# Kernel tuning notes

Hardware: AMD Instinct MI355X
Metric: run time of the kernel (lower is better)

The kernel has to match this reference:

```python
import jax, jax.numpy as jnp
import numpy as np

B, N, E = 8, 50000, 400000
DIMS = [4, 64, 64, 3]
K = 3
EPS = 1e-5
NEG_SLOPE = 0.01


def _gcn_norm(edge_index, num_nodes):
    # TAGConv uses gcn_norm with unit edge weights and add_self_loops=False.
    row, col = edge_index[0], edge_index[1]
    w = jnp.ones(row.shape[0], dtype=jnp.float32)
    deg = jax.ops.segment_sum(w, col, num_segments=num_nodes)  # in-degree at target
    dis = jnp.where(deg > 0, jnp.power(jnp.maximum(deg, 1.0), -0.5), 0.0)
    return dis[row] * dis[col]  # [E]


def _tag_conv(x, W, b, row, col, norm, num_nodes):
    # x: [B, N, Fin]; W: [K+1, Fin, Fout]; b: [Fout]
    out = jnp.einsum('bnf,fg->bng', x, W[0])
    h = x
    for k in range(1, W.shape[0]):
        msg = h[:, row, :] * norm[None, :, None]            # [B, E, Fin] gather
        h = jnp.zeros((x.shape[0], num_nodes, x.shape[2]), x.dtype).at[:, col, :].add(msg)  # scatter-add
        out = out + jnp.einsum('bnf,fg->bng', h, W[k])
    return out + b


def _batchnorm(x2d, gamma, beta):
    # training-mode BatchNorm1d over batch dim (biased variance, eps=1e-5)
    mean = jnp.mean(x2d, axis=0)
    var = jnp.mean(jnp.square(x2d - mean), axis=0)
    return gamma * (x2d - mean) * jax.lax.rsqrt(var + EPS) + beta


def _leaky_relu(x):
    return jnp.where(x >= 0, x, NEG_SLOPE * x)


def setup_inputs() -> dict:
    key = jax.random.key(0)
    ks = jax.random.split(key, 12)
    inp = {}
    inp['x'] = jax.random.normal(ks[0], (B, N, DIMS[0]), dtype=jnp.float32)
    inp['edge_index'] = jax.random.randint(ks[1], (2, E), 0, N, dtype=jnp.int64)
    inp['val_min'] = jax.random.uniform(ks[2], (N, 3), dtype=jnp.float32) - 1.5
    inp['val_max'] = jax.random.uniform(ks[3], (N, 3), dtype=jnp.float32) + 0.5
    for l in range(3):
        fin, fout = DIMS[l], DIMS[l + 1]
        scale = 1.0 / np.sqrt(fin)
        inp[f'W{l}'] = jax.random.uniform(ks[4 + l], (K + 1, fin, fout), minval=-scale, maxval=scale, dtype=jnp.float32)
        inp[f'b{l}'] = jnp.zeros((fout,), jnp.float32)
    for l in range(2):
        inp[f'gamma{l}'] = jnp.ones((N * DIMS[l + 1],), jnp.float32)
        inp[f'beta{l}'] = jnp.zeros((N * DIMS[l + 1],), jnp.float32)
    return inp


def reference(x, edge_index, val_min, val_max, W0, b0, W1, b1, W2, b2,
              gamma0, beta0, gamma1, beta1):
    row, col = edge_index[0], edge_index[1]
    norm = _gcn_norm(edge_index, N)
    Ws = [W0, W1, W2]
    bs = [b0, b1, b2]
    gammas = [gamma0, gamma1]
    betas = [beta0, beta1]
    out = x
    for layer in range(2):  # num_layers - 1 hidden layers
        out = _tag_conv(out, Ws[layer], bs[layer], row, col, norm, N)
        d = DIMS[layer + 1]
        out = _batchnorm(out.reshape(-1, N * d), gammas[layer], betas[layer]).reshape(-1, N, d)
        out = _leaky_relu(out)
    out = _tag_conv(out, Ws[2], bs[2], row, col, norm, N)  # [B, N, 3]
    # non_linearity: gamma = min + (max - min) / (1 + exp(U))
    return val_min[None] + (val_max - val_min)[None] / (1.0 + jnp.exp(out))
```

## Files before the change

### kernel.cpp

```cpp
#include <hip/hip_runtime.h>
#include <math.h>

constexpr int B = 8;
constexpr int N = 50000;
constexpr int E = 400000;
constexpr int NH = 25000;
constexpr float BN_EPS = 1e-5f;
constexpr float NEG = 0.01f;


__device__ __forceinline__ unsigned clamp_src(int s) {
    unsigned u = (unsigned)s;
    return (u < (unsigned)N) ? u : 0u;
}

__device__ __forceinline__ unsigned pack_bf16(float a, float b) {
    unsigned ua = __float_as_uint(a);
    unsigned ub = __float_as_uint(b);
    ua = (ua + 0x7FFFu + ((ua >> 16) & 1u)) >> 16;
    ub = (ub + 0x7FFFu + ((ub >> 16) & 1u)) >> 16;
    return (ub << 16) | (ua & 0xFFFFu);
}
__device__ __forceinline__ float unpack_lo(unsigned u) { return __uint_as_float(u << 16); }
__device__ __forceinline__ float unpack_hi(unsigned u) { return __uint_as_float(u & 0xFFFF0000u); }

__device__ __forceinline__ void store_row64_bf(uint4* p, const float acc[64]) {
#pragma unroll
    for (int q = 0; q < 8; ++q) {
        uint4 v;
        v.x = pack_bf16(acc[q * 8 + 0], acc[q * 8 + 1]);
        v.y = pack_bf16(acc[q * 8 + 2], acc[q * 8 + 3]);
        v.z = pack_bf16(acc[q * 8 + 4], acc[q * 8 + 5]);
        v.w = pack_bf16(acc[q * 8 + 6], acc[q * 8 + 7]);
        p[q] = v;
    }
}


__global__ __launch_bounds__(256) void deg2_kernel(const int* __restrict__ row, const int* __restrict__ col,
                                                   float* __restrict__ deg, int* __restrict__ deg_lo) {
    int e = blockIdx.x * blockDim.x + threadIdx.x;
    if (e >= E) return;
    unsigned r = clamp_src(row[e]), c = clamp_src(col[e]);
    atomicAdd(&deg[c], 1.0f);
    if (r < (unsigned)NH) atomicAdd(&deg_lo[c], 1);
}

__global__ __launch_bounds__(256) void scan1_kernel(const float* __restrict__ deg,
                                                    int* __restrict__ part, int* __restrict__ bsum) {
    __shared__ int sm[4];
    int i = blockIdx.x * blockDim.x + threadIdx.x;
    int v = (i < N) ? (int)deg[i] : 0;
    int lane = threadIdx.x & 63, wv = threadIdx.x >> 6;
    int x = v;
#pragma unroll
    for (int off = 1; off < 64; off <<= 1) {
        int t = __shfl_up(x, off);
        if (lane >= off) x += t;
    }
    if (lane == 63) sm[wv] = x;
    __syncthreads();
    int add = 0;
#pragma unroll
    for (int w = 0; w < 4; ++w) if (w < wv) add += sm[w];
    if (i < N) part[i] = x - v + add;
    if (threadIdx.x == blockDim.x - 1) bsum[blockIdx.x] = x + add;
}

__global__ __launch_bounds__(256) void scan2_kernel(const int* __restrict__ bsum, int* __restrict__ boff,
                                                    int nb, int* __restrict__ rowptr) {
    __shared__ int sm[4];
    int i = threadIdx.x;
    int v = (i < nb) ? bsum[i] : 0;
    int lane = i & 63, wv = i >> 6;
    int x = v;
#pragma unroll
    for (int off = 1; off < 64; off <<= 1) {
        int t = __shfl_up(x, off);
        if (lane >= off) x += t;
    }
    if (lane == 63) sm[wv] = x;
    __syncthreads();
    int add = 0;
#pragma unroll
    for (int w = 0; w < 4; ++w) if (w < wv) add += sm[w];
    if (i < nb) boff[i] = x - v + add;
    if (i == 0) rowptr[N] = E;
}

__global__ __launch_bounds__(256) void scan3_kernel(const int* __restrict__ part, const int* __restrict__ boff,
                                                    int* __restrict__ rowptr) {
    int i = blockIdx.x * blockDim.x + threadIdx.x;
    if (i < N) rowptr[i] = part[i] + boff[blockIdx.x];
}

__global__ __launch_bounds__(256) void fill_kernel(const int* __restrict__ row, const int* __restrict__ col,
                                                   const int* __restrict__ rowptr, const int* __restrict__ deg_lo,
                                                   int* __restrict__ cur_lo, int* __restrict__ cur_hi,
                                                   int* __restrict__ csr_src) {
    int e = blockIdx.x * blockDim.x + threadIdx.x;
    if (e >= E) return;
    unsigned r = clamp_src(row[e]), c = clamp_src(col[e]);
    unsigned p;
    if (r < (unsigned)NH)
        p = (unsigned)(rowptr[c] + atomicAdd(&cur_lo[c], 1));
    else
        p = (unsigned)(rowptr[c] + deg_lo[c] + atomicAdd(&cur_hi[c], 1));
    if (p >= (unsigned)E) p = E - 1;
    csr_src[p] = (int)r;
}

__global__ __launch_bounds__(256) void dis_kernel(float* __restrict__ deg) {
    int i = blockIdx.x * blockDim.x + threadIdx.x;
    if (i < N) {
        float d = deg[i];
        deg[i] = (d > 0.f) ? rsqrtf(d) : 0.f;
    }
}


template<bool INBF>
__global__ __launch_bounds__(256) void xprop_kernel(const void* __restrict__ xin, const int* __restrict__ rowptr,
                                                    const int* __restrict__ csr_src, const float* __restrict__ dis,
                                                    uint2* __restrict__ xout) {
    int b = blockIdx.x & 7;
    int n = (blockIdx.x >> 3) * blockDim.x + threadIdx.x;
    if (n >= N) return;
    float a0 = 0.f, a1 = 0.f, a2 = 0.f, a3 = 0.f;
    int beg = rowptr[n], end = rowptr[n + 1];
    if (beg < 0) beg = 0;
    if (end > E) end = E;
    for (int i = beg; i < end; ++i) {
        unsigned s = clamp_src(csr_src[i]);
        float w = dis[s];
        if constexpr (!INBF) {
            float4 v = *((const float4*)xin + (size_t)b * N + s);
            a0 = fmaf(w, v.x, a0); a1 = fmaf(w, v.y, a1);
            a2 = fmaf(w, v.z, a2); a3 = fmaf(w, v.w, a3);
        } else {
            uint2 v = *((const uint2*)xin + (size_t)b * N + s);
            a0 = fmaf(w, unpack_lo(v.x), a0); a1 = fmaf(w, unpack_hi(v.x), a1);
            a2 = fmaf(w, unpack_lo(v.y), a2); a3 = fmaf(w, unpack_hi(v.y), a3);
        }
    }
    float dn = dis[n];
    uint2 o;
    o.x = pack_bf16(a0 * dn, a1 * dn);
    o.y = pack_bf16(a2 * dn, a3 * dn);
    xout[(size_t)b * N + n] = o;
}


__device__ __forceinline__ void load_xv(const float4* __restrict__ x0, const uint2* __restrict__ x1,
                                        const uint2* __restrict__ x2, const uint2* __restrict__ x3,
                                        size_t ro, float xv[16]) {
    float4 v = x0[ro];
    xv[0] = v.x; xv[1] = v.y; xv[2] = v.z; xv[3] = v.w;
    uint2 u1 = x1[ro], u2 = x2[ro], u3 = x3[ro];
    xv[4] = unpack_lo(u1.x); xv[5] = unpack_hi(u1.x); xv[6] = unpack_lo(u1.y); xv[7] = unpack_hi(u1.y);
    xv[8] = unpack_lo(u2.x); xv[9] = unpack_hi(u2.x); xv[10] = unpack_lo(u2.y); xv[11] = unpack_hi(u2.y);
    xv[12] = unpack_lo(u3.x); xv[13] = unpack_hi(u3.x); xv[14] = unpack_lo(u3.y); xv[15] = unpack_hi(u3.y);
}


__global__ __launch_bounds__(256) void build_h1_kernel(const float4* __restrict__ x0, const uint2* __restrict__ x1,
                                                       const uint2* __restrict__ x2, const uint2* __restrict__ x3,
                                                       const float* __restrict__ W0,
                                                       const float* __restrict__ gamma, const float* __restrict__ beta,
                                                       uint4* __restrict__ h1) {
    int gid = blockIdx.x * blockDim.x + threadIdx.x;
    int node = gid >> 6;
    int lane = gid & 63;
    int fg = lane >> 3, b = lane & 7;
    if (node >= N) return;
    size_t ro = (size_t)b * N + node;
    float xv[16];
    load_xv(x0, x1, x2, x3, ro, xv);
    float z[8];
#pragma unroll
    for (int j = 0; j < 8; ++j) z[j] = 0.f;
#pragma unroll
    for (int kf = 0; kf < 16; ++kf) {
        const float* wr = W0 + kf * 64 + fg * 8;
        float4 wa = *(const float4*)wr;
        float4 wb = *(const float4*)(wr + 4);
        float xs = xv[kf];
        z[0] = fmaf(xs, wa.x, z[0]); z[1] = fmaf(xs, wa.y, z[1]);
        z[2] = fmaf(xs, wa.z, z[2]); z[3] = fmaf(xs, wa.w, z[3]);
        z[4] = fmaf(xs, wb.x, z[4]); z[5] = fmaf(xs, wb.y, z[5]);
        z[6] = fmaf(xs, wb.z, z[6]); z[7] = fmaf(xs, wb.w, z[7]);
    }
    const float* gp = gamma + (size_t)node * 64 + fg * 8;
    const float* bp = beta + (size_t)node * 64 + fg * 8;
    float h[8];
#pragma unroll
    for (int j = 0; j < 8; ++j) {
        float v = z[j];
        float s = v, s2 = v * v;
        s += __shfl_xor(s, 1);  s += __shfl_xor(s, 2);  s += __shfl_xor(s, 4);
        s2 += __shfl_xor(s2, 1); s2 += __shfl_xor(s2, 2); s2 += __shfl_xor(s2, 4);
        float mean = s * 0.125f;
        float var = fmaf(-mean, mean, s2 * 0.125f);
        float rs = rsqrtf(var + BN_EPS);
        float o = fmaf(gp[j] * rs, v - mean, bp[j]);
        h[j] = (o >= 0.f) ? o : NEG * o;
    }
    uint4 o;
    o.x = pack_bf16(h[0], h[1]);
    o.y = pack_bf16(h[2], h[3]);
    o.z = pack_bf16(h[4], h[5]);
    o.w = pack_bf16(h[6], h[7]);
    h1[ro * 8 + fg] = o;
}


__device__ __forceinline__ void fma_row(float acc[64], float w, const uint4 r[8]) {
#pragma unroll
    for (int q = 0; q < 8; ++q) {
        uint4 v = r[q];
        acc[q * 8 + 0] = fmaf(w, unpack_lo(v.x), acc[q * 8 + 0]);
        acc[q * 8 + 1] = fmaf(w, unpack_hi(v.x), acc[q * 8 + 1]);
        acc[q * 8 + 2] = fmaf(w, unpack_lo(v.y), acc[q * 8 + 2]);
        acc[q * 8 + 3] = fmaf(w, unpack_hi(v.y), acc[q * 8 + 3]);
        acc[q * 8 + 4] = fmaf(w, unpack_lo(v.z), acc[q * 8 + 4]);
        acc[q * 8 + 5] = fmaf(w, unpack_hi(v.z), acc[q * 8 + 5]);
        acc[q * 8 + 6] = fmaf(w, unpack_lo(v.w), acc[q * 8 + 6]);
        acc[q * 8 + 7] = fmaf(w, unpack_hi(v.w), acc[q * 8 + 7]);
    }
}

__device__ __forceinline__ void gather64_bf(const uint4* __restrict__ ub8, int beg, int end,
                                            const int* __restrict__ csr_src, const float* __restrict__ dis,
                                            float acc[64]) {
    if (beg < 0) beg = 0;
    if (end > E) end = E;
    int i = beg;
    for (; i + 1 < end; i += 2) {
        unsigned s0 = clamp_src(csr_src[i]);
        unsigned s1 = clamp_src(csr_src[i + 1]);
        float w0 = dis[s0], w1 = dis[s1];
        const uint4* p0 = ub8 + (size_t)s0 * 8;
        const uint4* p1 = ub8 + (size_t)s1 * 8;
        uint4 r0[8], r1[8];
#pragma unroll
        for (int q = 0; q < 8; ++q) r0[q] = p0[q];
#pragma unroll
        for (int q = 0; q < 8; ++q) r1[q] = p1[q];
        fma_row(acc, w0, r0);
        fma_row(acc, w1, r1);
    }
    if (i < end) {
        unsigned s0 = clamp_src(csr_src[i]);
        float w0 = dis[s0];
        const uint4* p0 = ub8 + (size_t)s0 * 8;
        uint4 r0[8];
#pragma unroll
        for (int q = 0; q < 8; ++q) r0[q] = p0[q];
        fma_row(acc, w0, r0);
    }
}

__device__ __forceinline__ void dense64_bf(const uint4* __restrict__ hp8, const float* __restrict__ W, float acc[64]) {
#pragma unroll 1
    for (int kk = 0; kk < 4; ++kk) {
        float hreg[16];
        uint4 va = hp8[kk * 2], vb = hp8[kk * 2 + 1];
        hreg[0] = unpack_lo(va.x); hreg[1] = unpack_hi(va.x);
        hreg[2] = unpack_lo(va.y); hreg[3] = unpack_hi(va.y);
        hreg[4] = unpack_lo(va.z); hreg[5] = unpack_hi(va.z);
        hreg[6] = unpack_lo(va.w); hreg[7] = unpack_hi(va.w);
        hreg[8] = unpack_lo(vb.x); hreg[9] = unpack_hi(vb.x);
        hreg[10] = unpack_lo(vb.y); hreg[11] = unpack_hi(vb.y);
        hreg[12] = unpack_lo(vb.z); hreg[13] = unpack_hi(vb.z);
        hreg[14] = unpack_lo(vb.w); hreg[15] = unpack_hi(vb.w);
        const float* Wp = W + kk * 16 * 64;
#pragma unroll
        for (int k = 0; k < 16; ++k) {
            float hv = hreg[k];
#pragma unroll
            for (int c = 0; c < 64; ++c)
                acc[c] = fmaf(hv, Wp[k * 64 + c], acc[c]);
        }
    }
}


template<int MODE>
__global__ __launch_bounds__(256) void hopM_kernel(const uint4* __restrict__ u_in, const int* __restrict__ rowptr,
                                                   const int* __restrict__ csr_src, const float* __restrict__ dis,
                                                   const uint4* __restrict__ h1, int b0, int bmask, int bshift,
                                                   const float* __restrict__ Wk, const float* __restrict__ bias,
                                                   uint4* __restrict__ u_out) {
    int bl = blockIdx.x & bmask;
    int n = (blockIdx.x >> bshift) * blockDim.x + threadIdx.x;
    if (n >= N) return;
    float acc[64];
#pragma unroll
    for (int f = 0; f < 64; ++f) acc[f] = 0.f;
    if constexpr (MODE > 0) {
        gather64_bf(u_in + (size_t)bl * N * 8, rowptr[n], rowptr[n + 1], csr_src, dis, acc);
        float dn = dis[n];
#pragma unroll
        for (int f = 0; f < 64; ++f) acc[f] *= dn;
    }
    if constexpr (MODE == 2) {
#pragma unroll
        for (int f = 0; f < 64; ++f) acc[f] += bias[f];
    }
    dense64_bf(h1 + ((size_t)(b0 + bl) * N + n) * 8, Wk, acc);
    store_row64_bf(u_out + ((size_t)bl * N + n) * 8, acc);
}


__global__ __launch_bounds__(256) void bn_project_kernel(const uint4* __restrict__ zlo, const uint4* __restrict__ zhi,
                                                         const float* __restrict__ gamma, const float* __restrict__ beta,
                                                         const float* __restrict__ W2, float* __restrict__ y) {
    int gid = blockIdx.x * blockDim.x + threadIdx.x;
    int node = gid >> 6;
    int lane = gid & 63;
    int fg = lane >> 3, b = lane & 7;
    if (node >= N) return;
    const uint4* zp = (b < 4) ? (zlo + ((size_t)b * N + node) * 8)
                              : (zhi + ((size_t)(b - 4) * N + node) * 8);
    uint4 v = zp[fg];
    float h[8] = {unpack_lo(v.x), unpack_hi(v.x), unpack_lo(v.y), unpack_hi(v.y),
                  unpack_lo(v.z), unpack_hi(v.z), unpack_lo(v.w), unpack_hi(v.w)};
    const float* gp = gamma + (size_t)node * 64 + fg * 8;
    const float* bp = beta + (size_t)node * 64 + fg * 8;
#pragma unroll
    for (int j = 0; j < 8; ++j) {
        float val = h[j];
        float s = val, s2 = val * val;
        s += __shfl_xor(s, 1);  s += __shfl_xor(s, 2);  s += __shfl_xor(s, 4);
        s2 += __shfl_xor(s2, 1); s2 += __shfl_xor(s2, 2); s2 += __shfl_xor(s2, 4);
        float mean = s * 0.125f;
        float var = fmaf(-mean, mean, s2 * 0.125f);
        float rs = rsqrtf(var + BN_EPS);
        float o = fmaf(gp[j] * rs, val - mean, bp[j]);
        h[j] = (o >= 0.f) ? o : NEG * o;
    }
    float p[12];
#pragma unroll
    for (int k = 0; k < 4; ++k) {
#pragma unroll
        for (int c = 0; c < 3; ++c) {
            float s = 0.f;
#pragma unroll
            for (int j = 0; j < 8; ++j)
                s = fmaf(h[j], W2[k * 192 + (fg * 8 + j) * 3 + c], s);
            p[k * 3 + c] = s;
        }
    }
#pragma unroll
    for (int t = 8; t < 64; t <<= 1) {
#pragma unroll
        for (int i = 0; i < 12; ++i)
            p[i] += __shfl_xor(p[i], t);
    }
    if (fg == 0) {
        size_t bn3 = ((size_t)b * N + node) * 3;
#pragma unroll
        for (int k = 0; k < 4; ++k)
#pragma unroll
            for (int c = 0; c < 3; ++c)
                y[(size_t)k * B * N * 3 + bn3 + c] = p[k * 3 + c];
    }
}


__global__ __launch_bounds__(256) void qprop_kernel(const float* __restrict__ vin, const int* __restrict__ rowptr,
                                                    const int* __restrict__ csr_src, const float* __restrict__ dis,
                                                    const float* __restrict__ add, float* __restrict__ vout) {
    int b = blockIdx.x & 7;
    int n = (blockIdx.x >> 3) * blockDim.x + threadIdx.x;
    if (n >= N) return;
    float a0 = 0.f, a1 = 0.f, a2 = 0.f;
    int beg = rowptr[n], end = rowptr[n + 1];
    if (beg < 0) beg = 0;
    if (end > E) end = E;
    const float* base = vin + (size_t)b * N * 3;
    for (int i = beg; i < end; ++i) {
        unsigned s = clamp_src(csr_src[i]);
        float w = dis[s];
        const float* p = base + (size_t)s * 3;
        a0 = fmaf(w, p[0], a0);
        a1 = fmaf(w, p[1], a1);
        a2 = fmaf(w, p[2], a2);
    }
    float dn = dis[n];
    const float* ap = add + ((size_t)b * N + n) * 3;
    float* op = vout + ((size_t)b * N + n) * 3;
    op[0] = fmaf(a0, dn, ap[0]);
    op[1] = fmaf(a1, dn, ap[1]);
    op[2] = fmaf(a2, dn, ap[2]);
}

__global__ __launch_bounds__(256) void qfinal_kernel(const float* __restrict__ vin, const int* __restrict__ rowptr,
                                                     const int* __restrict__ csr_src, const float* __restrict__ dis,
                                                     const float* __restrict__ y0, const float* __restrict__ b2,
                                                     const float* __restrict__ vmin, const float* __restrict__ vmax,
                                                     float* __restrict__ out) {
    int b = blockIdx.x & 7;
    int n = (blockIdx.x >> 3) * blockDim.x + threadIdx.x;
    if (n >= N) return;
    float a0 = 0.f, a1 = 0.f, a2 = 0.f;
    int beg = rowptr[n], end = rowptr[n + 1];
    if (beg < 0) beg = 0;
    if (end > E) end = E;
    const float* base = vin + (size_t)b * N * 3;
    for (int i = beg; i < end; ++i) {
        unsigned s = clamp_src(csr_src[i]);
        float w = dis[s];
        const float* p = base + (size_t)s * 3;
        a0 = fmaf(w, p[0], a0);
        a1 = fmaf(w, p[1], a1);
        a2 = fmaf(w, p[2], a2);
    }
    float dn = dis[n];
    size_t bn3 = ((size_t)b * N + n) * 3;
    const float* yp = y0 + bn3;
    float g0 = fmaf(a0, dn, yp[0]) + b2[0];
    float g1 = fmaf(a1, dn, yp[1]) + b2[1];
    float g2 = fmaf(a2, dn, yp[2]) + b2[2];
    float mn0 = vmin[n * 3 + 0], mx0 = vmax[n * 3 + 0];
    float mn1 = vmin[n * 3 + 1], mx1 = vmax[n * 3 + 1];
    float mn2 = vmin[n * 3 + 2], mx2 = vmax[n * 3 + 2];
    float* op = out + bn3;
    op[0] = mn0 + (mx0 - mn0) / (1.f + expf(g0));
    op[1] = mn1 + (mx1 - mn1) / (1.f + expf(g1));
    op[2] = mn2 + (mx2 - mn2) / (1.f + expf(g2));
}


extern "C" void kernel_launch(void* const* d_in, const int* in_sizes, int n_in,
                              void* d_out, int out_size, void* d_ws, size_t ws_size,
                              hipStream_t stream) {
    const float* x      = (const float*)d_in[0];
    const int*   ei     = (const int*)d_in[1];
    const int*   rowi   = ei;
    const int*   coli   = ei + E;
    const float* vmin   = (const float*)d_in[2];
    const float* vmax   = (const float*)d_in[3];
    const float* W0     = (const float*)d_in[4];
    const float* W1     = (const float*)d_in[6];
    const float* b1v    = (const float*)d_in[7];
    const float* W2     = (const float*)d_in[8];
    const float* b2v    = (const float*)d_in[9];
    const float* gamma0 = (const float*)d_in[10];
    const float* beta0  = (const float*)d_in[11];
    const float* gamma1 = (const float*)d_in[12];
    const float* beta1  = (const float*)d_in[13];
    float* out = (float*)d_out;

    const size_t BN3  = (size_t)B * N * 3;
    const size_t H1FL = (size_t)B * N * 32;
    const size_t UCFL = (size_t)4 * N * 32;
    const size_t XBFL = (size_t)B * N * 2;

    auto rnd = [](size_t nf) { return (nf + 63) & ~(size_t)63; };
    size_t off = 0;
    auto alloc = [&](size_t nfloats) -> float* {
        float* p = (float*)d_ws + off;
        off += rnd(nfloats);
        return p;
    };
    float* deg     = alloc(N);
    int*   deg_lo  = (int*)alloc(N);
    int*   rowptr  = (int*)alloc(N + 1);
    int*   part    = (int*)alloc(N);
    int*   bsum    = (int*)alloc(256);
    int*   boff    = (int*)alloc(256);
    int*   cur_lo  = (int*)alloc(N);
    int*   cur_hi  = (int*)alloc(N);
    int*   csr_src = (int*)alloc(E);
    float* h1      = alloc(H1FL);

    const size_t avail_fl = ws_size / 4;
    const size_t need_full = off + 2 * H1FL + 4096;
    bool full = (avail_fl >= need_full);

    float *uA, *uB, *uC = nullptr;
    if (full) {
        uA = alloc(H1FL);
        uB = alloc(H1FL);
    } else {
        uA = alloc(UCFL);
        uB = alloc(UCFL);
        uC = alloc(UCFL);
    }
    uint2* xb1 = (uint2*)uA;
    uint2* xb2 = (uint2*)((float*)uA + XBFL);
    uint2* xb3 = (uint2*)((float*)uA + 2 * XBFL);
    float* y   = h1;
    float* v_a = h1 + rnd(4 * BN3);
    float* v_b = v_a + rnd(BN3);

    const int GE  = (E + 255) / 256;
    const int GN  = (N + 255) / 256;
    const int GB8 = GN * 8;
    const int GH4 = GN * 4;
    const int GW  = (N * 64) / 256;
    dim3 blk(256);

    hipMemsetAsync(deg, 0, N * sizeof(float), stream);
    hipMemsetAsync(deg_lo, 0, N * sizeof(int), stream);
    hipMemsetAsync(cur_lo, 0, N * sizeof(int), stream);
    hipMemsetAsync(cur_hi, 0, N * sizeof(int), stream);
    deg2_kernel<<<GE, blk, 0, stream>>>(rowi, coli, deg, deg_lo);
    scan1_kernel<<<GN, blk, 0, stream>>>(deg, part, bsum);
    scan2_kernel<<<1, blk, 0, stream>>>(bsum, boff, GN, rowptr);
    scan3_kernel<<<GN, blk, 0, stream>>>(part, boff, rowptr);
    fill_kernel<<<GE, blk, 0, stream>>>(rowi, coli, rowptr, deg_lo, cur_lo, cur_hi, csr_src);
    dis_kernel<<<GN, blk, 0, stream>>>(deg);
    const float* dis = deg;

    xprop_kernel<false><<<GB8, blk, 0, stream>>>(x,   rowptr, csr_src, dis, xb1);
    xprop_kernel<true><<<GB8, blk, 0, stream>>>(xb1, rowptr, csr_src, dis, xb2);
    xprop_kernel<true><<<GB8, blk, 0, stream>>>(xb2, rowptr, csr_src, dis, xb3);
    build_h1_kernel<<<GW, blk, 0, stream>>>((const float4*)x, xb1, xb2, xb3, W0, gamma0, beta0, (uint4*)h1);

    const uint4* H1 = (const uint4*)h1;
    if (full) {
        hopM_kernel<0><<<GB8, blk, 0, stream>>>(nullptr, rowptr, csr_src, dis, H1, 0, 7, 3,
                                                W1 + 3 * 4096, nullptr, (uint4*)uA);
        hopM_kernel<1><<<GB8, blk, 0, stream>>>((const uint4*)uA, rowptr, csr_src, dis, H1, 0, 7, 3,
                                                W1 + 2 * 4096, nullptr, (uint4*)uB);
        hopM_kernel<1><<<GB8, blk, 0, stream>>>((const uint4*)uB, rowptr, csr_src, dis, H1, 0, 7, 3,
                                                W1 + 1 * 4096, nullptr, (uint4*)uA);
        hopM_kernel<2><<<GB8, blk, 0, stream>>>((const uint4*)uA, rowptr, csr_src, dis, H1, 0, 7, 3,
                                                W1, b1v, (uint4*)uB);
        bn_project_kernel<<<GW, blk, 0, stream>>>((const uint4*)uB, (const uint4*)(uB + 4 * (size_t)N * 32),
                                                  gamma1, beta1, W2, y);
    } else {
        hopM_kernel<0><<<GB8, blk, 0, stream>>>(nullptr, rowptr, csr_src, dis, H1, 0, 7, 3,
                                                W1 + 3 * 4096, nullptr, (uint4*)uA);
        hopM_kernel<1><<<GH4, blk, 0, stream>>>((const uint4*)uA, rowptr, csr_src, dis, H1, 0, 3, 2,
                                                W1 + 2 * 4096, nullptr, (uint4*)uC);
        hopM_kernel<1><<<GH4, blk, 0, stream>>>((const uint4*)uC, rowptr, csr_src, dis, H1, 0, 3, 2,
                                                W1 + 1 * 4096, nullptr, (uint4*)uA);
        hopM_kernel<2><<<GH4, blk, 0, stream>>>((const uint4*)uA, rowptr, csr_src, dis, H1, 0, 3, 2,
                                                W1, b1v, (uint4*)uC);
        hopM_kernel<1><<<GH4, blk, 0, stream>>>((const uint4*)uB, rowptr, csr_src, dis, H1, 4, 3, 2,
                                                W1 + 2 * 4096, nullptr, (uint4*)uA);
        hopM_kernel<1><<<GH4, blk, 0, stream>>>((const uint4*)uA, rowptr, csr_src, dis, H1, 4, 3, 2,
                                                W1 + 1 * 4096, nullptr, (uint4*)uB);
        hopM_kernel<2><<<GH4, blk, 0, stream>>>((const uint4*)uB, rowptr, csr_src, dis, H1, 4, 3, 2,
                                                W1, b1v, (uint4*)uA);
        bn_project_kernel<<<GW, blk, 0, stream>>>((const uint4*)uC, (const uint4*)uA,
                                                  gamma1, beta1, W2, y);
    }

    qprop_kernel<<<GB8, blk, 0, stream>>>(y + 3 * BN3, rowptr, csr_src, dis, y + 2 * BN3, v_a);
    qprop_kernel<<<GB8, blk, 0, stream>>>(v_a, rowptr, csr_src, dis, y + 1 * BN3, v_b);
    qfinal_kernel<<<GB8, blk, 0, stream>>>(v_b, rowptr, csr_src, dis, y, b2v, vmin, vmax, out);
}
```

Baseline: 926.3 us.

## Use wave-cooperative coalesced gather and LDS transpose in hop kernels

Replaces the thread-per-node hop kernel, where each thread gathers whole 128-byte neighbor rows, with a wave-cooperative version. Each half-wave gathers one node's 64 bf16 features as 32 coalesced dwords per neighbor edge, then transposes through LDS so each thread still runs the per-node 64x64 dense update. The h1 load and output store also go through the LDS transpose to keep global accesses coalesced. In exchange the neighbor loop becomes serial per half-wave with one dword per lane, the gathered sum is rounded to bf16 before the degree scaling, and each block now uses about 33 KB of LDS.

```diff
diff --git a/kernel.cpp b/kernel.cpp
--- a/kernel.cpp
+++ b/kernel.cpp
@@ -23,18 +23,6 @@
 }
 __device__ __forceinline__ float unpack_lo(unsigned u) { return __uint_as_float(u << 16); }
 __device__ __forceinline__ float unpack_hi(unsigned u) { return __uint_as_float(u & 0xFFFF0000u); }
-
-__device__ __forceinline__ void store_row64_bf(uint4* p, const float acc[64]) {
-#pragma unroll
-    for (int q = 0; q < 8; ++q) {
-        uint4 v;
-        v.x = pack_bf16(acc[q * 8 + 0], acc[q * 8 + 1]);
-        v.y = pack_bf16(acc[q * 8 + 2], acc[q * 8 + 3]);
-        v.z = pack_bf16(acc[q * 8 + 4], acc[q * 8 + 5]);
-        v.w = pack_bf16(acc[q * 8 + 6], acc[q * 8 + 7]);
-        p[q] = v;
-    }
-}
 
 
 __global__ __launch_bounds__(256) void deg2_kernel(const int* __restrict__ row, const int* __restrict__ col,
@@ -214,101 +202,91 @@
 }
 
 
-__device__ __forceinline__ void fma_row(float acc[64], float w, const uint4 r[8]) {
-#pragma unroll
-    for (int q = 0; q < 8; ++q) {
-        uint4 v = r[q];
-        acc[q * 8 + 0] = fmaf(w, unpack_lo(v.x), acc[q * 8 + 0]);
-        acc[q * 8 + 1] = fmaf(w, unpack_hi(v.x), acc[q * 8 + 1]);
-        acc[q * 8 + 2] = fmaf(w, unpack_lo(v.y), acc[q * 8 + 2]);
-        acc[q * 8 + 3] = fmaf(w, unpack_hi(v.y), acc[q * 8 + 3]);
-        acc[q * 8 + 4] = fmaf(w, unpack_lo(v.z), acc[q * 8 + 4]);
-        acc[q * 8 + 5] = fmaf(w, unpack_hi(v.z), acc[q * 8 + 5]);
-        acc[q * 8 + 6] = fmaf(w, unpack_lo(v.w), acc[q * 8 + 6]);
-        acc[q * 8 + 7] = fmaf(w, unpack_hi(v.w), acc[q * 8 + 7]);
-    }
-}
-
-__device__ __forceinline__ void gather64_bf(const uint4* __restrict__ ub8, int beg, int end,
-                                            const int* __restrict__ csr_src, const float* __restrict__ dis,
-                                            float acc[64]) {
-    if (beg < 0) beg = 0;
-    if (end > E) end = E;
-    int i = beg;
-    for (; i + 1 < end; i += 2) {
-        unsigned s0 = clamp_src(csr_src[i]);
-        unsigned s1 = clamp_src(csr_src[i + 1]);
-        float w0 = dis[s0], w1 = dis[s1];
-        const uint4* p0 = ub8 + (size_t)s0 * 8;
-        const uint4* p1 = ub8 + (size_t)s1 * 8;
-        uint4 r0[8], r1[8];
-#pragma unroll
-        for (int q = 0; q < 8; ++q) r0[q] = p0[q];
-#pragma unroll
-        for (int q = 0; q < 8; ++q) r1[q] = p1[q];
-        fma_row(acc, w0, r0);
-        fma_row(acc, w1, r1);
-    }
-    if (i < end) {
-        unsigned s0 = clamp_src(csr_src[i]);
-        float w0 = dis[s0];
-        const uint4* p0 = ub8 + (size_t)s0 * 8;
-        uint4 r0[8];
-#pragma unroll
-        for (int q = 0; q < 8; ++q) r0[q] = p0[q];
-        fma_row(acc, w0, r0);
-    }
-}
-
-__device__ __forceinline__ void dense64_bf(const uint4* __restrict__ hp8, const float* __restrict__ W, float acc[64]) {
+template<int MODE>
+__global__ __launch_bounds__(256, 4) void hopW_kernel(const unsigned* __restrict__ u_in, const int* __restrict__ rowptr,
+                                                      const int* __restrict__ csr_src, const float* __restrict__ dis,
+                                                      const unsigned* __restrict__ h1, int b0, int bmask, int bshift,
+                                                      const float* __restrict__ Wk, const float* __restrict__ bias,
+                                                      unsigned* __restrict__ u_out) {
+    __shared__ unsigned lds[4][32][65];
+    int bl = blockIdx.x & bmask;
+    int w = threadIdx.x >> 6;
+    int lane = threadIdx.x & 63;
+    int half = lane >> 5, l = lane & 31;
+    int wbase = (blockIdx.x >> bshift) * 256 + w * 64;
+    unsigned (*L)[65] = lds[w];
+
+    if constexpr (MODE > 0) {
+        const unsigned* ub = u_in + (size_t)bl * N * 32;
+        for (int j = 0; j < 32; ++j) {
+            int n = wbase + 2 * j + half;
+            float a0 = 0.f, a1 = 0.f;
+            if (n < N) {
+                int beg = rowptr[n], end = rowptr[n + 1];
+                if (beg < 0) beg = 0;
+                if (end > E) end = E;
+                for (int i = beg; i < end; ++i) {
+                    unsigned s = clamp_src(csr_src[i]);
+                    float wgt = dis[s];
+                    unsigned v = ub[(size_t)s * 32 + l];
+                    a0 = fmaf(wgt, unpack_lo(v), a0);
+                    a1 = fmaf(wgt, unpack_hi(v), a1);
+                }
+            }
+            L[l][2 * j + half] = pack_bf16(a0, a1);
+        }
+    }
+
+    int node = wbase + lane;
+    int nodec = (node < N) ? node : N - 1;
+    float acc[64];
+    if constexpr (MODE > 0) {
+        float dn = dis[nodec];
+#pragma unroll
+        for (int q = 0; q < 32; ++q) {
+            unsigned u = L[q][lane];
+            acc[2 * q]     = unpack_lo(u) * dn;
+            acc[2 * q + 1] = unpack_hi(u) * dn;
+        }
+    } else {
+#pragma unroll
+        for (int f = 0; f < 64; ++f) acc[f] = 0.f;
+    }
+    if constexpr (MODE == 2) {
+#pragma unroll
+        for (int f = 0; f < 64; ++f) acc[f] += bias[f];
+    }
+
+    {
+        const unsigned* hb = h1 + (size_t)(b0 + bl) * N * 32;
+        for (int j = 0; j < 32; ++j) {
+            int n = wbase + 2 * j + half;
+            unsigned hv = (n < N) ? hb[(size_t)n * 32 + l] : 0u;
+            L[l][2 * j + half] = hv;
+        }
+    }
+
 #pragma unroll 1
-    for (int kk = 0; kk < 4; ++kk) {
-        float hreg[16];
-        uint4 va = hp8[kk * 2], vb = hp8[kk * 2 + 1];
-        hreg[0] = unpack_lo(va.x); hreg[1] = unpack_hi(va.x);
-        hreg[2] = unpack_lo(va.y); hreg[3] = unpack_hi(va.y);
-        hreg[4] = unpack_lo(va.z); hreg[5] = unpack_hi(va.z);
-        hreg[6] = unpack_lo(va.w); hreg[7] = unpack_hi(va.w);
-        hreg[8] = unpack_lo(vb.x); hreg[9] = unpack_hi(vb.x);
-        hreg[10] = unpack_lo(vb.y); hreg[11] = unpack_hi(vb.y);
-        hreg[12] = unpack_lo(vb.z); hreg[13] = unpack_hi(vb.z);
-        hreg[14] = unpack_lo(vb.w); hreg[15] = unpack_hi(vb.w);
-        const float* Wp = W + kk * 16 * 64;
-#pragma unroll
-        for (int k = 0; k < 16; ++k) {
-            float hv = hreg[k];
-#pragma unroll
-            for (int c = 0; c < 64; ++c)
-                acc[c] = fmaf(hv, Wp[k * 64 + c], acc[c]);
-        }
-    }
-}
-
-
-template<int MODE>
-__global__ __launch_bounds__(256) void hopM_kernel(const uint4* __restrict__ u_in, const int* __restrict__ rowptr,
-                                                   const int* __restrict__ csr_src, const float* __restrict__ dis,
-                                                   const uint4* __restrict__ h1, int b0, int bmask, int bshift,
-                                                   const float* __restrict__ Wk, const float* __restrict__ bias,
-                                                   uint4* __restrict__ u_out) {
-    int bl = blockIdx.x & bmask;
-    int n = (blockIdx.x >> bshift) * blockDim.x + threadIdx.x;
-    if (n >= N) return;
-    float acc[64];
-#pragma unroll
-    for (int f = 0; f < 64; ++f) acc[f] = 0.f;
-    if constexpr (MODE > 0) {
-        gather64_bf(u_in + (size_t)bl * N * 8, rowptr[n], rowptr[n + 1], csr_src, dis, acc);
-        float dn = dis[n];
-#pragma unroll
-        for (int f = 0; f < 64; ++f) acc[f] *= dn;
-    }
-    if constexpr (MODE == 2) {
-#pragma unroll
-        for (int f = 0; f < 64; ++f) acc[f] += bias[f];
-    }
-    dense64_bf(h1 + ((size_t)(b0 + bl) * N + n) * 8, Wk, acc);
-    store_row64_bf(u_out + ((size_t)bl * N + n) * 8, acc);
+    for (int k2 = 0; k2 < 32; ++k2) {
+        unsigned hu = L[k2][lane];
+        float h0 = unpack_lo(hu), h1f = unpack_hi(hu);
+        const float* w0 = Wk + 2 * k2 * 64;
+#pragma unroll
+        for (int c = 0; c < 64; ++c)
+            acc[c] = fmaf(h0, w0[c], acc[c]);
+#pragma unroll
+        for (int c = 0; c < 64; ++c)
+            acc[c] = fmaf(h1f, w0[64 + c], acc[c]);
+    }
+
+#pragma unroll
+    for (int q = 0; q < 32; ++q)
+        L[q][lane] = pack_bf16(acc[2 * q], acc[2 * q + 1]);
+    unsigned* ob = u_out + (size_t)bl * N * 32;
+    for (int j = 0; j < 32; ++j) {
+        int n = wbase + 2 * j + half;
+        if (n < N) ob[(size_t)n * 32 + l] = L[l][2 * j + half];
+    }
 }
 
 
@@ -519,33 +497,33 @@
     xprop_kernel<true><<<GB8, blk, 0, stream>>>(xb2, rowptr, csr_src, dis, xb3);
     build_h1_kernel<<<GW, blk, 0, stream>>>((const float4*)x, xb1, xb2, xb3, W0, gamma0, beta0, (uint4*)h1);
 
-    const uint4* H1 = (const uint4*)h1;
+    const unsigned* H1 = (const unsigned*)h1;
     if (full) {
-        hopM_kernel<0><<<GB8, blk, 0, stream>>>(nullptr, rowptr, csr_src, dis, H1, 0, 7, 3,
-                                                W1 + 3 * 4096, nullptr, (uint4*)uA);
-        hopM_kernel<1><<<GB8, blk, 0, stream>>>((const uint4*)uA, rowptr, csr_src, dis, H1, 0, 7, 3,
-                                                W1 + 2 * 4096, nullptr, (uint4*)uB);
-        hopM_kernel<1><<<GB8, blk, 0, stream>>>((const uint4*)uB, rowptr, csr_src, dis, H1, 0, 7, 3,
-                                                W1 + 1 * 4096, nullptr, (uint4*)uA);
-        hopM_kernel<2><<<GB8, blk, 0, stream>>>((const uint4*)uA, rowptr, csr_src, dis, H1, 0, 7, 3,
-                                                W1, b1v, (uint4*)uB);
+        hopW_kernel<0><<<GB8, blk, 0, stream>>>(nullptr, rowptr, csr_src, dis, H1, 0, 7, 3,
+                                                W1 + 3 * 4096, nullptr, (unsigned*)uA);
+        hopW_kernel<1><<<GB8, blk, 0, stream>>>((const unsigned*)uA, rowptr, csr_src, dis, H1, 0, 7, 3,
+                                                W1 + 2 * 4096, nullptr, (unsigned*)uB);
+        hopW_kernel<1><<<GB8, blk, 0, stream>>>((const unsigned*)uB, rowptr, csr_src, dis, H1, 0, 7, 3,
+                                                W1 + 1 * 4096, nullptr, (unsigned*)uA);
+        hopW_kernel<2><<<GB8, blk, 0, stream>>>((const unsigned*)uA, rowptr, csr_src, dis, H1, 0, 7, 3,
+                                                W1, b1v, (unsigned*)uB);
         bn_project_kernel<<<GW, blk, 0, stream>>>((const uint4*)uB, (const uint4*)(uB + 4 * (size_t)N * 32),
                                                   gamma1, beta1, W2, y);
     } else {
-        hopM_kernel<0><<<GB8, blk, 0, stream>>>(nullptr, rowptr, csr_src, dis, H1, 0, 7, 3,
-                                                W1 + 3 * 4096, nullptr, (uint4*)uA);
-        hopM_kernel<1><<<GH4, blk, 0, stream>>>((const uint4*)uA, rowptr, csr_src, dis, H1, 0, 3, 2,
-                                                W1 + 2 * 4096, nullptr, (uint4*)uC);
-        hopM_kernel<1><<<GH4, blk, 0, stream>>>((const uint4*)uC, rowptr, csr_src, dis, H1, 0, 3, 2,
-                                                W1 + 1 * 4096, nullptr, (uint4*)uA);
-        hopM_kernel<2><<<GH4, blk, 0, stream>>>((const uint4*)uA, rowptr, csr_src, dis, H1, 0, 3, 2,
-                                                W1, b1v, (uint4*)uC);
-        hopM_kernel<1><<<GH4, blk, 0, stream>>>((const uint4*)uB, rowptr, csr_src, dis, H1, 4, 3, 2,
-                                                W1 + 2 * 4096, nullptr, (uint4*)uA);
-        hopM_kernel<1><<<GH4, blk, 0, stream>>>((const uint4*)uA, rowptr, csr_src, dis, H1, 4, 3, 2,
-                                                W1 + 1 * 4096, nullptr, (uint4*)uB);
-        hopM_kernel<2><<<GH4, blk, 0, stream>>>((const uint4*)uB, rowptr, csr_src, dis, H1, 4, 3, 2,
-                                                W1, b1v, (uint4*)uA);
+        hopW_kernel<0><<<GB8, blk, 0, stream>>>(nullptr, rowptr, csr_src, dis, H1, 0, 7, 3,
+                                                W1 + 3 * 4096, nullptr, (unsigned*)uA);
+        hopW_kernel<1><<<GH4, blk, 0, stream>>>((const unsigned*)uA, rowptr, csr_src, dis, H1, 0, 3, 2,
+                                                W1 + 2 * 4096, nullptr, (unsigned*)uC);
+        hopW_kernel<1><<<GH4, blk, 0, stream>>>((const unsigned*)uC, rowptr, csr_src, dis, H1, 0, 3, 2,
+                                                W1 + 1 * 4096, nullptr, (unsigned*)uA);
+        hopW_kernel<2><<<GH4, blk, 0, stream>>>((const unsigned*)uA, rowptr, csr_src, dis, H1, 0, 3, 2,
+                                                W1, b1v, (unsigned*)uC);
+        hopW_kernel<1><<<GH4, blk, 0, stream>>>((const unsigned*)uB, rowptr, csr_src, dis, H1, 4, 3, 2,
+                                                W1 + 2 * 4096, nullptr, (unsigned*)uA);
+        hopW_kernel<1><<<GH4, blk, 0, stream>>>((const unsigned*)uA, rowptr, csr_src, dis, H1, 4, 3, 2,
+                                                W1 + 1 * 4096, nullptr, (unsigned*)uB);
+        hopW_kernel<2><<<GH4, blk, 0, stream>>>((const unsigned*)uB, rowptr, csr_src, dis, H1, 4, 3, 2,
+                                                W1, b1v, (unsigned*)uA);
         bn_project_kernel<<<GW, blk, 0, stream>>>((const uint4*)uC, (const uint4*)uA,
                                                   gamma1, beta1, W2, y);
     }
```

Measured after the change: 1.721 ms. 85.8% more time.

## Split hop kernel feature work across waves and stage output through LDS

Applied to the files above, without the earlier changes.

The per-node 64-feature hop kernel becomes a 128-node block where two waves each handle half of the 64 output features. Each thread now holds 32 accumulators instead of 64, and launch bounds are raised to target more resident waves. Outputs are staged through padded shared memory so global stores are coalesced. Smaller fixes are bundled in: the dis kernel is fused into scan3, the four memsets become one, and the BN shuffle loops are batched. The cost is that each node's gather indices and h1 row are loaded twice, once per half.

```diff
diff --git a/kernel.cpp b/kernel.cpp
--- a/kernel.cpp
+++ b/kernel.cpp
@@ -23,18 +23,6 @@
 }
 __device__ __forceinline__ float unpack_lo(unsigned u) { return __uint_as_float(u << 16); }
 __device__ __forceinline__ float unpack_hi(unsigned u) { return __uint_as_float(u & 0xFFFF0000u); }
-
-__device__ __forceinline__ void store_row64_bf(uint4* p, const float acc[64]) {
-#pragma unroll
-    for (int q = 0; q < 8; ++q) {
-        uint4 v;
-        v.x = pack_bf16(acc[q * 8 + 0], acc[q * 8 + 1]);
-        v.y = pack_bf16(acc[q * 8 + 2], acc[q * 8 + 3]);
-        v.z = pack_bf16(acc[q * 8 + 4], acc[q * 8 + 5]);
-        v.w = pack_bf16(acc[q * 8 + 6], acc[q * 8 + 7]);
-        p[q] = v;
-    }
-}
 
 
 __global__ __launch_bounds__(256) void deg2_kernel(const int* __restrict__ row, const int* __restrict__ col,
@@ -88,10 +76,14 @@
     if (i == 0) rowptr[N] = E;
 }
 
-__global__ __launch_bounds__(256) void scan3_kernel(const int* __restrict__ part, const int* __restrict__ boff,
-                                                    int* __restrict__ rowptr) {
+__global__ __launch_bounds__(256) void scan3_dis_kernel(const int* __restrict__ part, const int* __restrict__ boff,
+                                                        int* __restrict__ rowptr, float* __restrict__ deg) {
     int i = blockIdx.x * blockDim.x + threadIdx.x;
-    if (i < N) rowptr[i] = part[i] + boff[blockIdx.x];
+    if (i < N) {
+        rowptr[i] = part[i] + boff[blockIdx.x];
+        float d = deg[i];
+        deg[i] = (d > 0.f) ? rsqrtf(d) : 0.f;
+    }
 }
 
 __global__ __launch_bounds__(256) void fill_kernel(const int* __restrict__ row, const int* __restrict__ col,
@@ -108,14 +100,6 @@
         p = (unsigned)(rowptr[c] + deg_lo[c] + atomicAdd(&cur_hi[c], 1));
     if (p >= (unsigned)E) p = E - 1;
     csr_src[p] = (int)r;
-}
-
-__global__ __launch_bounds__(256) void dis_kernel(float* __restrict__ deg) {
-    int i = blockIdx.x * blockDim.x + threadIdx.x;
-    if (i < N) {
-        float d = deg[i];
-        deg[i] = (d > 0.f) ? rsqrtf(d) : 0.f;
-    }
 }
 
 
@@ -190,19 +174,26 @@
         z[4] = fmaf(xs, wb.x, z[4]); z[5] = fmaf(xs, wb.y, z[5]);
         z[6] = fmaf(xs, wb.z, z[6]); z[7] = fmaf(xs, wb.w, z[7]);
     }
+    float s[8], s2[8];
+#pragma unroll
+    for (int j = 0; j < 8; ++j) { s[j] = z[j]; s2[j] = z[j] * z[j]; }
+#pragma unroll
+    for (int off = 1; off < 8; off <<= 1) {
+#pragma unroll
+        for (int j = 0; j < 8; ++j) {
+            s[j] += __shfl_xor(s[j], off);
+            s2[j] += __shfl_xor(s2[j], off);
+        }
+    }
     const float* gp = gamma + (size_t)node * 64 + fg * 8;
     const float* bp = beta + (size_t)node * 64 + fg * 8;
     float h[8];
 #pragma unroll
     for (int j = 0; j < 8; ++j) {
-        float v = z[j];
-        float s = v, s2 = v * v;
-        s += __shfl_xor(s, 1);  s += __shfl_xor(s, 2);  s += __shfl_xor(s, 4);
-        s2 += __shfl_xor(s2, 1); s2 += __shfl_xor(s2, 2); s2 += __shfl_xor(s2, 4);
-        float mean = s * 0.125f;
-        float var = fmaf(-mean, mean, s2 * 0.125f);
+        float mean = s[j] * 0.125f;
+        float var = fmaf(-mean, mean, s2[j] * 0.125f);
         float rs = rsqrtf(var + BN_EPS);
-        float o = fmaf(gp[j] * rs, v - mean, bp[j]);
+        float o = fmaf(gp[j] * rs, z[j] - mean, bp[j]);
         h[j] = (o >= 0.f) ? o : NEG * o;
     }
     uint4 o;
@@ -214,101 +205,108 @@
 }
 
 
-__device__ __forceinline__ void fma_row(float acc[64], float w, const uint4 r[8]) {
-#pragma unroll
-    for (int q = 0; q < 8; ++q) {
-        uint4 v = r[q];
-        acc[q * 8 + 0] = fmaf(w, unpack_lo(v.x), acc[q * 8 + 0]);
-        acc[q * 8 + 1] = fmaf(w, unpack_hi(v.x), acc[q * 8 + 1]);
-        acc[q * 8 + 2] = fmaf(w, unpack_lo(v.y), acc[q * 8 + 2]);
-        acc[q * 8 + 3] = fmaf(w, unpack_hi(v.y), acc[q * 8 + 3]);
-        acc[q * 8 + 4] = fmaf(w, unpack_lo(v.z), acc[q * 8 + 4]);
-        acc[q * 8 + 5] = fmaf(w, unpack_hi(v.z), acc[q * 8 + 5]);
-        acc[q * 8 + 6] = fmaf(w, unpack_lo(v.w), acc[q * 8 + 6]);
-        acc[q * 8 + 7] = fmaf(w, unpack_hi(v.w), acc[q * 8 + 7]);
-    }
-}
-
-__device__ __forceinline__ void gather64_bf(const uint4* __restrict__ ub8, int beg, int end,
-                                            const int* __restrict__ csr_src, const float* __restrict__ dis,
-                                            float acc[64]) {
-    if (beg < 0) beg = 0;
-    if (end > E) end = E;
-    int i = beg;
-    for (; i + 1 < end; i += 2) {
-        unsigned s0 = clamp_src(csr_src[i]);
-        unsigned s1 = clamp_src(csr_src[i + 1]);
-        float w0 = dis[s0], w1 = dis[s1];
-        const uint4* p0 = ub8 + (size_t)s0 * 8;
-        const uint4* p1 = ub8 + (size_t)s1 * 8;
-        uint4 r0[8], r1[8];
-#pragma unroll
-        for (int q = 0; q < 8; ++q) r0[q] = p0[q];
-#pragma unroll
-        for (int q = 0; q < 8; ++q) r1[q] = p1[q];
-        fma_row(acc, w0, r0);
-        fma_row(acc, w1, r1);
-    }
-    if (i < end) {
-        unsigned s0 = clamp_src(csr_src[i]);
-        float w0 = dis[s0];
-        const uint4* p0 = ub8 + (size_t)s0 * 8;
-        uint4 r0[8];
-#pragma unroll
-        for (int q = 0; q < 8; ++q) r0[q] = p0[q];
-        fma_row(acc, w0, r0);
-    }
-}
-
-__device__ __forceinline__ void dense64_bf(const uint4* __restrict__ hp8, const float* __restrict__ W, float acc[64]) {
-#pragma unroll 1
-    for (int kk = 0; kk < 4; ++kk) {
-        float hreg[16];
-        uint4 va = hp8[kk * 2], vb = hp8[kk * 2 + 1];
-        hreg[0] = unpack_lo(va.x); hreg[1] = unpack_hi(va.x);
-        hreg[2] = unpack_lo(va.y); hreg[3] = unpack_hi(va.y);
-        hreg[4] = unpack_lo(va.z); hreg[5] = unpack_hi(va.z);
-        hreg[6] = unpack_lo(va.w); hreg[7] = unpack_hi(va.w);
-        hreg[8] = unpack_lo(vb.x); hreg[9] = unpack_hi(vb.x);
-        hreg[10] = unpack_lo(vb.y); hreg[11] = unpack_hi(vb.y);
-        hreg[12] = unpack_lo(vb.z); hreg[13] = unpack_hi(vb.z);
-        hreg[14] = unpack_lo(vb.w); hreg[15] = unpack_hi(vb.w);
-        const float* Wp = W + kk * 16 * 64;
-#pragma unroll
-        for (int k = 0; k < 16; ++k) {
-            float hv = hreg[k];
-#pragma unroll
-            for (int c = 0; c < 64; ++c)
-                acc[c] = fmaf(hv, Wp[k * 64 + c], acc[c]);
-        }
-    }
-}
-
-
 template<int MODE>
-__global__ __launch_bounds__(256) void hopM_kernel(const uint4* __restrict__ u_in, const int* __restrict__ rowptr,
-                                                   const int* __restrict__ csr_src, const float* __restrict__ dis,
-                                                   const uint4* __restrict__ h1, int b0, int bmask, int bshift,
-                                                   const float* __restrict__ Wk, const float* __restrict__ bias,
-                                                   uint4* __restrict__ u_out) {
+__global__ __launch_bounds__(256, 6) void hopG_kernel(const unsigned* __restrict__ u_in, const int* __restrict__ rowptr,
+                                                      const int* __restrict__ csr_src, const float* __restrict__ dis,
+                                                      const uint4* __restrict__ h1, int b0, int bmask, int bshift,
+                                                      const float* __restrict__ Wk, const float* __restrict__ bias,
+                                                      uint4* __restrict__ u_out) {
+    __shared__ unsigned lds[128 * 33];
     int bl = blockIdx.x & bmask;
-    int n = (blockIdx.x >> bshift) * blockDim.x + threadIdx.x;
-    if (n >= N) return;
-    float acc[64];
-#pragma unroll
-    for (int f = 0; f < 64; ++f) acc[f] = 0.f;
+    int g  = blockIdx.x >> bshift;
+    int tid = threadIdx.x;
+    int w = tid >> 6, lane = tid & 63;
+    int sub = w & 1, half = w >> 1;
+    int n = g * 128 + sub * 64 + lane;
+    int nc = (n < N) ? n : N - 1;
+
+    float acc[32];
+#pragma unroll
+    for (int c = 0; c < 32; ++c) acc[c] = 0.f;
+
     if constexpr (MODE > 0) {
-        gather64_bf(u_in + (size_t)bl * N * 8, rowptr[n], rowptr[n + 1], csr_src, dis, acc);
-        float dn = dis[n];
-#pragma unroll
-        for (int f = 0; f < 64; ++f) acc[f] *= dn;
+        const uint4* U4 = (const uint4*)u_in;
+        int beg = rowptr[nc], end = rowptr[nc + 1];
+        if (beg < 0) beg = 0;
+        if (end > E) end = E;
+        if (n >= N) end = beg;
+        for (int i = beg; i < end; ++i) {
+            unsigned s = clamp_src(csr_src[i]);
+            float wgt = dis[s];
+            const uint4* ur = U4 + ((size_t)bl * N + s) * 8 + half * 4;
+            uint4 r0 = ur[0], r1 = ur[1], r2 = ur[2], r3 = ur[3];
+            acc[0]  = fmaf(wgt, unpack_lo(r0.x), acc[0]);  acc[1]  = fmaf(wgt, unpack_hi(r0.x), acc[1]);
+            acc[2]  = fmaf(wgt, unpack_lo(r0.y), acc[2]);  acc[3]  = fmaf(wgt, unpack_hi(r0.y), acc[3]);
+            acc[4]  = fmaf(wgt, unpack_lo(r0.z), acc[4]);  acc[5]  = fmaf(wgt, unpack_hi(r0.z), acc[5]);
+            acc[6]  = fmaf(wgt, unpack_lo(r0.w), acc[6]);  acc[7]  = fmaf(wgt, unpack_hi(r0.w), acc[7]);
+            acc[8]  = fmaf(wgt, unpack_lo(r1.x), acc[8]);  acc[9]  = fmaf(wgt, unpack_hi(r1.x), acc[9]);
+            acc[10] = fmaf(wgt, unpack_lo(r1.y), acc[10]); acc[11] = fmaf(wgt, unpack_hi(r1.y), acc[11]);
+            acc[12] = fmaf(wgt, unpack_lo(r1.z), acc[12]); acc[13] = fmaf(wgt, unpack_hi(r1.z), acc[13]);
+            acc[14] = fmaf(wgt, unpack_lo(r1.w), acc[14]); acc[15] = fmaf(wgt, unpack_hi(r1.w), acc[15]);
+            acc[16] = fmaf(wgt, unpack_lo(r2.x), acc[16]); acc[17] = fmaf(wgt, unpack_hi(r2.x), acc[17]);
+            acc[18] = fmaf(wgt, unpack_lo(r2.y), acc[18]); acc[19] = fmaf(wgt, unpack_hi(r2.y), acc[19]);
+            acc[20] = fmaf(wgt, unpack_lo(r2.z), acc[20]); acc[21] = fmaf(wgt, unpack_hi(r2.z), acc[21]);
+            acc[22] = fmaf(wgt, unpack_lo(r2.w), acc[22]); acc[23] = fmaf(wgt, unpack_hi(r2.w), acc[23]);
+            acc[24] = fmaf(wgt, unpack_lo(r3.x), acc[24]); acc[25] = fmaf(wgt, unpack_hi(r3.x), acc[25]);
+            acc[26] = fmaf(wgt, unpack_lo(r3.y), acc[26]); acc[27] = fmaf(wgt, unpack_hi(r3.y), acc[27]);
+            acc[28] = fmaf(wgt, unpack_lo(r3.z), acc[28]); acc[29] = fmaf(wgt, unpack_hi(r3.z), acc[29]);
+            acc[30] = fmaf(wgt, unpack_lo(r3.w), acc[30]); acc[31] = fmaf(wgt, unpack_hi(r3.w), acc[31]);
+        }
+        float dn = dis[nc];
+#pragma unroll
+        for (int c = 0; c < 32; ++c) acc[c] *= dn;
     }
     if constexpr (MODE == 2) {
-#pragma unroll
-        for (int f = 0; f < 64; ++f) acc[f] += bias[f];
-    }
-    dense64_bf(h1 + ((size_t)(b0 + bl) * N + n) * 8, Wk, acc);
-    store_row64_bf(u_out + ((size_t)bl * N + n) * 8, acc);
+        const float* bp = bias + half * 32;
+#pragma unroll
+        for (int c = 0; c < 32; ++c) acc[c] += bp[c];
+    }
+
+    {
+        const uint4* hr = h1 + ((size_t)(b0 + bl) * N + nc) * 8;
+#pragma unroll 2
+        for (int kk = 0; kk < 8; ++kk) {
+            uint4 hv = hr[kk];
+            unsigned hs[4] = {hv.x, hv.y, hv.z, hv.w};
+#pragma unroll
+            for (int t = 0; t < 4; ++t) {
+                int k = kk * 8 + t * 2;
+                float h0 = unpack_lo(hs[t]);
+                float h1f = unpack_hi(hs[t]);
+                const float* w0 = Wk + k * 64 + half * 32;
+                const float* w1 = w0 + 64;
+#pragma unroll
+                for (int c = 0; c < 32; ++c) acc[c] = fmaf(h0, w0[c], acc[c]);
+#pragma unroll
+                for (int c = 0; c < 32; ++c) acc[c] = fmaf(h1f, w1[c], acc[c]);
+            }
+        }
+    }
+
+    {
+        unsigned* Lr = lds + (sub * 64 + lane) * 33 + half * 16;
+#pragma unroll
+        for (int q = 0; q < 16; ++q)
+            Lr[q] = pack_bf16(acc[2 * q], acc[2 * q + 1]);
+    }
+    __syncthreads();
+
+    {
+        int f = tid * 4;
+        int row = f >> 3;
+        int nout = g * 128 + row;
+        if (nout < N) {
+            const unsigned* Ls = lds + row * 33 + (f & 7) * 4;
+            uint4* op = u_out + ((size_t)bl * N + (size_t)g * 128) * 8 + f;
+#pragma unroll
+            for (int j = 0; j < 4; ++j) {
+                uint4 v;
+                v.x = Ls[j * 4 + 0]; v.y = Ls[j * 4 + 1];
+                v.z = Ls[j * 4 + 2]; v.w = Ls[j * 4 + 3];
+                op[j] = v;
+            }
+        }
+    }
 }
 
 
@@ -325,18 +323,25 @@
     uint4 v = zp[fg];
     float h[8] = {unpack_lo(v.x), unpack_hi(v.x), unpack_lo(v.y), unpack_hi(v.y),
                   unpack_lo(v.z), unpack_hi(v.z), unpack_lo(v.w), unpack_hi(v.w)};
+    float s[8], s2[8];
+#pragma unroll
+    for (int j = 0; j < 8; ++j) { s[j] = h[j]; s2[j] = h[j] * h[j]; }
+#pragma unroll
+    for (int off = 1; off < 8; off <<= 1) {
+#pragma unroll
+        for (int j = 0; j < 8; ++j) {
+            s[j] += __shfl_xor(s[j], off);
+            s2[j] += __shfl_xor(s2[j], off);
+        }
+    }
     const float* gp = gamma + (size_t)node * 64 + fg * 8;
     const float* bp = beta + (size_t)node * 64 + fg * 8;
 #pragma unroll
     for (int j = 0; j < 8; ++j) {
-        float val = h[j];
-        float s = val, s2 = val * val;
-        s += __shfl_xor(s, 1);  s += __shfl_xor(s, 2);  s += __shfl_xor(s, 4);
-        s2 += __shfl_xor(s2, 1); s2 += __shfl_xor(s2, 2); s2 += __shfl_xor(s2, 4);
-        float mean = s * 0.125f;
-        float var = fmaf(-mean, mean, s2 * 0.125f);
+        float mean = s[j] * 0.125f;
+        float var = fmaf(-mean, mean, s2[j] * 0.125f);
         float rs = rsqrtf(var + BN_EPS);
-        float o = fmaf(gp[j] * rs, val - mean, bp[j]);
+        float o = fmaf(gp[j] * rs, h[j] - mean, bp[j]);
         h[j] = (o >= 0.f) ? o : NEG * o;
     }
     float p[12];
@@ -344,11 +349,11 @@
     for (int k = 0; k < 4; ++k) {
 #pragma unroll
         for (int c = 0; c < 3; ++c) {
-            float s = 0.f;
+            float sv = 0.f;
 #pragma unroll
             for (int j = 0; j < 8; ++j)
-                s = fmaf(h[j], W2[k * 192 + (fg * 8 + j) * 3 + c], s);
-            p[k * 3 + c] = s;
+                sv = fmaf(h[j], W2[k * 192 + (fg * 8 + j) * 3 + c], sv);
+            p[k * 3 + c] = sv;
         }
     }
 #pragma unroll
@@ -466,12 +471,13 @@
     };
     float* deg     = alloc(N);
     int*   deg_lo  = (int*)alloc(N);
+    int*   cur_lo  = (int*)alloc(N);
+    int*   cur_hi  = (int*)alloc(N);
+    size_t zero_bytes = (size_t)4 * rnd(N) * 4;
     int*   rowptr  = (int*)alloc(N + 1);
     int*   part    = (int*)alloc(N);
     int*   bsum    = (int*)alloc(256);
     int*   boff    = (int*)alloc(256);
-    int*   cur_lo  = (int*)alloc(N);
-    int*   cur_hi  = (int*)alloc(N);
     int*   csr_src = (int*)alloc(E);
     float* h1      = alloc(H1FL);
 
@@ -498,20 +504,16 @@
     const int GE  = (E + 255) / 256;
     const int GN  = (N + 255) / 256;
     const int GB8 = GN * 8;
-    const int GH4 = GN * 4;
     const int GW  = (N * 64) / 256;
+    const int NG  = (N + 127) / 128;
     dim3 blk(256);
 
-    hipMemsetAsync(deg, 0, N * sizeof(float), stream);
-    hipMemsetAsync(deg_lo, 0, N * sizeof(int), stream);
-    hipMemsetAsync(cur_lo, 0, N * sizeof(int), stream);
-    hipMemsetAsync(cur_hi, 0, N * sizeof(int), stream);
+    hipMemsetAsync(deg, 0, zero_bytes, stream);
     deg2_kernel<<<GE, blk, 0, stream>>>(rowi, coli, deg, deg_lo);
     scan1_kernel<<<GN, blk, 0, stream>>>(deg, part, bsum);
     scan2_kernel<<<1, blk, 0, stream>>>(bsum, boff, GN, rowptr);
-    scan3_kernel<<<GN, blk, 0, stream>>>(part, boff, rowptr);
+    scan3_dis_kernel<<<GN, blk, 0, stream>>>(part, boff, rowptr, deg);
     fill_kernel<<<GE, blk, 0, stream>>>(rowi, coli, rowptr, deg_lo, cur_lo, cur_hi, csr_src);
-    dis_kernel<<<GN, blk, 0, stream>>>(deg);
     const float* dis = deg;
 
     xprop_kernel<false><<<GB8, blk, 0, stream>>>(x,   rowptr, csr_src, dis, xb1);
@@ -521,31 +523,31 @@
 
     const uint4* H1 = (const uint4*)h1;
     if (full) {
-        hopM_kernel<0><<<GB8, blk, 0, stream>>>(nullptr, rowptr, csr_src, dis, H1, 0, 7, 3,
-                                                W1 + 3 * 4096, nullptr, (uint4*)uA);
-        hopM_kernel<1><<<GB8, blk, 0, stream>>>((const uint4*)uA, rowptr, csr_src, dis, H1, 0, 7, 3,
-                                                W1 + 2 * 4096, nullptr, (uint4*)uB);
-        hopM_kernel<1><<<GB8, blk, 0, stream>>>((const uint4*)uB, rowptr, csr_src, dis, H1, 0, 7, 3,
-                                                W1 + 1 * 4096, nullptr, (uint4*)uA);
-        hopM_kernel<2><<<GB8, blk, 0, stream>>>((const uint4*)uA, rowptr, csr_src, dis, H1, 0, 7, 3,
-                                                W1, b1v, (uint4*)uB);
+        hopG_kernel<0><<<NG * 8, blk, 0, stream>>>(nullptr, rowptr, csr_src, dis, H1, 0, 7, 3,
+                                                   W1 + 3 * 4096, nullptr, (uint4*)uA);
+        hopG_kernel<1><<<NG * 8, blk, 0, stream>>>((const unsigned*)uA, rowptr, csr_src, dis, H1, 0, 7, 3,
+                                                   W1 + 2 * 4096, nullptr, (uint4*)uB);
+        hopG_kernel<1><<<NG * 8, blk, 0, stream>>>((const unsigned*)uB, rowptr, csr_src, dis, H1, 0, 7, 3,
+                                                   W1 + 1 * 4096, nullptr, (uint4*)uA);
+        hopG_kernel<2><<<NG * 8, blk, 0, stream>>>((const unsigned*)uA, rowptr, csr_src, dis, H1, 0, 7, 3,
+                                                   W1, b1v, (uint4*)uB);
         bn_project_kernel<<<GW, blk, 0, stream>>>((const uint4*)uB, (const uint4*)(uB + 4 * (size_t)N * 32),
                                                   gamma1, beta1, W2, y);
     } else {
-        hopM_kernel<0><<<GB8, blk, 0, stream>>>(nullptr, rowptr, csr_src, dis, H1, 0, 7, 3,
-                                                W1 + 3 * 4096, nullptr, (uint4*)uA);
-        hopM_kernel<1><<<GH4, blk, 0, stream>>>((const uint4*)uA, rowptr, csr_src, dis, H1, 0, 3, 2,
-                                                W1 + 2 * 4096, nullptr, (uint4*)uC);
-        hopM_kernel<1><<<GH4, blk, 0, stream>>>((const uint4*)uC, rowptr, csr_src, dis, H1, 0, 3, 2,
-                                                W1 + 1 * 4096, nullptr, (uint4*)uA);
-        hopM_kernel<2><<<GH4, blk, 0, stream>>>((const uint4*)uA, rowptr, csr_src, dis, H1, 0, 3, 2,
-                                                W1, b1v, (uint4*)uC);
-        hopM_kernel<1><<<GH4, blk, 0, stream>>>((const uint4*)uB, rowptr, csr_src, dis, H1, 4, 3, 2,
-                                                W1 + 2 * 4096, nullptr, (uint4*)uA);
-        hopM_kernel<1><<<GH4, blk, 0, stream>>>((const uint4*)uA, rowptr, csr_src, dis, H1, 4, 3, 2,
-                                                W1 + 1 * 4096, nullptr, (uint4*)uB);
-        hopM_kernel<2><<<GH4, blk, 0, stream>>>((const uint4*)uB, rowptr, csr_src, dis, H1, 4, 3, 2,
-                                                W1, b1v, (uint4*)uA);
+        hopG_kernel<0><<<NG * 8, blk, 0, stream>>>(nullptr, rowptr, csr_src, dis, H1, 0, 7, 3,
+                                                   W1 + 3 * 4096, nullptr, (uint4*)uA);
+        hopG_kernel<1><<<NG * 4, blk, 0, stream>>>((const unsigned*)uA, rowptr, csr_src, dis, H1, 0, 3, 2,
+                                                   W1 + 2 * 4096, nullptr, (uint4*)uC);
+        hopG_kernel<1><<<NG * 4, blk, 0, stream>>>((const unsigned*)uC, rowptr, csr_src, dis, H1, 0, 3, 2,
+                                                   W1 + 1 * 4096, nullptr, (uint4*)uA);
+        hopG_kernel<2><<<NG * 4, blk, 0, stream>>>((const unsigned*)uA, rowptr, csr_src, dis, H1, 0, 3, 2,
+                                                   W1, b1v, (uint4*)uC);
+        hopG_kernel<1><<<NG * 4, blk, 0, stream>>>((const unsigned*)uB, rowptr, csr_src, dis, H1, 4, 3, 2,
+                                                   W1 + 2 * 4096, nullptr, (uint4*)uA);
+        hopG_kernel<1><<<NG * 4, blk, 0, stream>>>((const unsigned*)uA, rowptr, csr_src, dis, H1, 4, 3, 2,
+                                                   W1 + 1 * 4096, nullptr, (uint4*)uB);
+        hopG_kernel<2><<<NG * 4, blk, 0, stream>>>((const unsigned*)uB, rowptr, csr_src, dis, H1, 4, 3, 2,
+                                                   W1, b1v, (uint4*)uA);
         bn_project_kernel<<<GW, blk, 0, stream>>>((const uint4*)uC, (const uint4*)uA,
                                                   gamma1, beta1, W2, y);
     }
```

After: 1.732 ms. +87.0%, slower.
